# Kernel optimization log

Measured on AMD Instinct MI355X. Metric: run time of the kernel, lower is better.

The kernel has to match this reference:

```python
import jax, jax.numpy as jnp
import numpy as np

N_NODES = 200_000
N_EDGES = 400_000
EMB_DIM = 128
HID_DIM = 24
N_TYPES = 8


def setup_inputs() -> dict:
    key = jax.random.key(0)
    k_emb, k_src, k_typ, k_w1, k_w2 = jax.random.split(key, 5)
    rgcn_emb = jax.random.normal(k_emb, (N_NODES, EMB_DIM), dtype=jnp.float32)
    edge_index = jax.random.randint(k_src, (2, N_EDGES), 0, N_NODES, dtype=jnp.int32)
    edge_type = jax.random.randint(k_typ, (N_EDGES,), 0, N_TYPES, dtype=jnp.int32)
    # per-edge-type 2-layer MLP params: Linear(2D->H), Linear(H->1)
    W1 = jax.random.normal(k_w1, (N_TYPES, 2 * EMB_DIM, HID_DIM), dtype=jnp.float32) * 0.05
    b1 = jnp.zeros((N_TYPES, HID_DIM), dtype=jnp.float32)
    W2 = jax.random.normal(k_w2, (N_TYPES, HID_DIM), dtype=jnp.float32) * 0.05
    b2 = jnp.zeros((N_TYPES,), dtype=jnp.float32)
    return {"rgcn_emb": rgcn_emb, "edge_index": edge_index, "edge_type": edge_type,
            "W1": W1, "b1": b1, "W2": W2, "b2": b2}


def reference(rgcn_emb, edge_index, edge_type, W1, b1, W2, b2):
    src, dst = edge_index[0], edge_index[1]
    # gather + concat: [E, 2D]
    edge_emb = jnp.concatenate([rgcn_emb[src], rgcn_emb[dst]], axis=-1)
    # dense per-type expert compute, then select by routing (MoE-style)
    h = jnp.einsum('ed,tdh->teh', edge_emb, W1) + b1[:, None, :]  # [T,E,H]
    h = jnp.where(h > 0, h, 0.01 * h)  # LeakyReLU(0.01)
    s = jnp.einsum('teh,th->te', h, W2) + b2[:, None]  # [T,E]
    onehot = jax.nn.one_hot(edge_type, N_TYPES, dtype=s.dtype)  # [E,T]
    scores = jnp.einsum('te,et->e', s, onehot)  # scatter-select per edge
    return (scores, rgcn_emb)
```

## Files before the change

kernel.cpp:

```cpp
#include <hip/hip_runtime.h>


typedef float f4 __attribute__((ext_vector_type(4)));

constexpr int N_NODES = 200000;
constexpr int N_EDGES = 400000;
constexpr int EMB_DIM = 128;
constexpr int HID     = 24;
constexpr int N_TYPES = 8;
constexpr int BLK     = 256;

constexpr int CHUNKS  = 128;
constexpr int CH_SZ   = N_EDGES / CHUNKS;
constexpr int MAX_PAD = N_EDGES + N_TYPES * (BLK - 1);
constexpr int SCORE_BLOCKS = (MAX_PAD + BLK - 1) / BLK;
constexpr int COPY_BLOCKS  = 1024;

constexpr int OFF_CC     = 0;
constexpr int OFF_COUNTS = OFF_CC + CHUNKS * N_TYPES;
constexpr int OFF_POFF   = OFF_COUNTS + N_TYPES;
constexpr int OFF_SORTED = OFF_POFF + N_TYPES;
constexpr size_t WS_NEED = (size_t)(OFF_SORTED + MAX_PAD) * sizeof(int);

__global__ __launch_bounds__(BLK) void hist_k(const int* __restrict__ etype,
                                              int* __restrict__ ws) {
    __shared__ int lc[N_TYPES];
    int b = blockIdx.x;
    if (threadIdx.x < N_TYPES) lc[threadIdx.x] = 0;
    __syncthreads();
    int e0 = b * CH_SZ;
    const int4* et4 = (const int4*)(etype + e0);
    for (int e = e0 + (int)threadIdx.x; e < e0 + CH_SZ; e += BLK)
        atomicAdd(&lc[etype[e]], 1);
    (void)et4;
    __syncthreads();
    if (threadIdx.x < N_TYPES)
        ws[OFF_CC + b * N_TYPES + threadIdx.x] = lc[threadIdx.x];
}

__global__ __launch_bounds__(BLK) void scatter_k(
        const int* __restrict__ etype, int* __restrict__ ws) {
    __shared__ int sbase[N_TYPES];
    __shared__ int tot[N_TYPES];
    __shared__ int mybase[N_TYPES];
    __shared__ int spoff[N_TYPES];
    __shared__ int lc[N_TYPES];
    int b = blockIdx.x;
    if (threadIdx.x < N_TYPES) {
        int t = threadIdx.x, s = 0, mb = 0;
        for (int c = 0; c < CHUNKS; ++c) {
            if (c == b) mb = s;
            s += ws[OFF_CC + c * N_TYPES + t];
        }
        tot[t] = s;
        mybase[t] = mb;
        lc[t] = 0;
    }
    __syncthreads();
    if (threadIdx.x == 0) {
        int off = 0;
        for (int t = 0; t < N_TYPES; ++t) {
            spoff[t] = off;
            off += ((tot[t] + BLK - 1) / BLK) * BLK;
        }
    }
    __syncthreads();
    if (threadIdx.x < N_TYPES) {
        sbase[threadIdx.x] = spoff[threadIdx.x] + mybase[threadIdx.x];
        if (b == 0) {
            ws[OFF_COUNTS + threadIdx.x] = tot[threadIdx.x];
            ws[OFF_POFF + threadIdx.x]   = spoff[threadIdx.x];
        }
    }
    __syncthreads();
    int e0 = b * CH_SZ;
    int* sorted = ws + OFF_SORTED;
    for (int e = e0 + (int)threadIdx.x; e < e0 + CH_SZ; e += BLK) {
        int t = etype[e];
        int r = atomicAdd(&lc[t], 1);
        sorted[sbase[t] + r] = e;
    }
}

__device__ __forceinline__ void do_copy(const float* __restrict__ emb,
                                        float* __restrict__ out, int cb, int nb) {
    const f4* s4 = (const f4*)emb;
    f4* o4 = (f4*)(out + N_EDGES);
    const int n4 = N_NODES * EMB_DIM / 4;
    for (int i = cb * BLK + (int)threadIdx.x; i < n4; i += nb * BLK) {
        f4 a = s4[i];
        __builtin_nontemporal_store(a, &o4[i]);
    }
}

__device__ __forceinline__ void half_mm(const f4* __restrict__ x4,
                                        const float* __restrict__ w,
                                        float acc[HID]) {
#pragma unroll 1
    for (int c = 0; c < 4; ++c) {
        f4 r[8];
#pragma unroll
        for (int k = 0; k < 8; ++k) r[k] = x4[c * 8 + k];
#pragma unroll
        for (int k = 0; k < 8; ++k) {
            const float* wp = w + (c * 32 + k * 4) * HID;
#pragma unroll
            for (int j = 0; j < HID; ++j) acc[j] = fmaf(r[k][0], wp[0 * HID + j], acc[j]);
#pragma unroll
            for (int j = 0; j < HID; ++j) acc[j] = fmaf(r[k][1], wp[1 * HID + j], acc[j]);
#pragma unroll
            for (int j = 0; j < HID; ++j) acc[j] = fmaf(r[k][2], wp[2 * HID + j], acc[j]);
#pragma unroll
            for (int j = 0; j < HID; ++j) acc[j] = fmaf(r[k][3], wp[3 * HID + j], acc[j]);
        }
    }
}

__global__ __launch_bounds__(BLK) void score32_k(
        const float* __restrict__ emb,
        const int* __restrict__ srci, const int* __restrict__ dsti,
        const int* __restrict__ ws,
        const float* __restrict__ W1, const float* __restrict__ b1,
        const float* __restrict__ W2, const float* __restrict__ b2,
        float* __restrict__ out) {
    int b = blockIdx.x;
    if (b >= SCORE_BLOCKS) {
        do_copy(emb, out, b - SCORE_BLOCKS, (int)gridDim.x - SCORE_BLOCKS);
        return;
    }
    int poff[N_TYPES], counts[N_TYPES];
#pragma unroll
    for (int t = 0; t < N_TYPES; ++t) {
        counts[t] = ws[OFF_COUNTS + t];
        poff[t]   = ws[OFF_POFF + t];
    }
    int off = poff[N_TYPES - 1] + ((counts[N_TYPES - 1] + BLK - 1) / BLK) * BLK;
    int slot0 = b * BLK;
    if (slot0 >= off) return;
    int t = 0;
#pragma unroll
    for (int i = 1; i < N_TYPES; ++i)
        if (slot0 >= poff[i]) t = i;
    t = __builtin_amdgcn_readfirstlane(t);
    int cnt = counts[t];
    int local = slot0 - poff[t] + (int)threadIdx.x;
    if (local >= cnt) return;
    const int* sorted = ws + OFF_SORTED;
    int e = sorted[slot0 + threadIdx.x];
    int s = srci[e], d = dsti[e];

    float acc[HID];
#pragma unroll
    for (int j = 0; j < HID; ++j) acc[j] = b1[t * HID + j];
    const float* W1t = W1 + (size_t)t * (2 * EMB_DIM * HID);
    half_mm((const f4*)(emb + (size_t)s * EMB_DIM), W1t, acc);
    half_mm((const f4*)(emb + (size_t)d * EMB_DIM), W1t + EMB_DIM * HID, acc);
    float sc = b2[t];
#pragma unroll
    for (int j = 0; j < HID; ++j) {
        float h = acc[j];
        h = (h > 0.f) ? h : 0.01f * h;
        sc = fmaf(h, W2[t * HID + j], sc);
    }
    out[e] = sc;
}

__global__ __launch_bounds__(BLK) void fallback_k(
        const float* __restrict__ emb,
        const int* __restrict__ srci, const int* __restrict__ dsti,
        const int* __restrict__ etype,
        const float* __restrict__ W1, const float* __restrict__ b1,
        const float* __restrict__ W2, const float* __restrict__ b2,
        float* __restrict__ out) {
    long long i0 = (long long)blockIdx.x * BLK + threadIdx.x;
    const f4* s4 = (const f4*)emb;
    f4* o4 = (f4*)(out + N_EDGES);
    const long long n4 = (long long)N_NODES * EMB_DIM / 4;
    for (long long i = i0; i < n4; i += (long long)gridDim.x * BLK)
        o4[i] = s4[i];
    for (int e = (int)i0; e < N_EDGES; e += gridDim.x * BLK) {
        int t = etype[e];
        int s = srci[e], d = dsti[e];
        float acc[HID];
#pragma unroll
        for (int j = 0; j < HID; ++j) acc[j] = b1[t * HID + j];
        const float* w = W1 + (size_t)t * 2 * EMB_DIM * HID;
        half_mm((const f4*)(emb + (size_t)s * EMB_DIM), w, acc);
        half_mm((const f4*)(emb + (size_t)d * EMB_DIM), w + EMB_DIM * HID, acc);
        float sc = b2[t];
#pragma unroll
        for (int j = 0; j < HID; ++j) {
            float h = acc[j];
            h = (h > 0.f) ? h : 0.01f * h;
            sc = fmaf(h, W2[t * HID + j], sc);
        }
        out[e] = sc;
    }
}

extern "C" void kernel_launch(void* const* d_in, const int* in_sizes, int n_in,
                              void* d_out, int out_size, void* d_ws, size_t ws_size,
                              hipStream_t stream) {
    const float* emb   = (const float*)d_in[0];
    const int*   eidx  = (const int*)d_in[1];
    const int*   etype = (const int*)d_in[2];
    const float* W1    = (const float*)d_in[3];
    const float* b1    = (const float*)d_in[4];
    const float* W2    = (const float*)d_in[5];
    const float* b2    = (const float*)d_in[6];
    float* out = (float*)d_out;
    const int* srci = eidx;
    const int* dsti = eidx + N_EDGES;

    if (ws_size >= WS_NEED) {
        int* ws = (int*)d_ws;
        hist_k<<<CHUNKS, BLK, 0, stream>>>(etype, ws);
        scatter_k<<<CHUNKS, BLK, 0, stream>>>(etype, ws);
        score32_k<<<SCORE_BLOCKS + COPY_BLOCKS, BLK, 0, stream>>>(
            emb, srci, dsti, ws, W1, b1, W2, b2, out);
    } else {
        fallback_k<<<2048, BLK, 0, stream>>>(emb, srci, dsti, etype, W1, b1, W2, b2, out);
    }
}
```

Before: 264.2 us.

## Split each edge's src/dst half-matmul across two threads, combine in shared memory

The scoring kernel now handles 128 edges per 256-thread block. The first half of the block multiplies the source embedding against the first half of W1, and the second half multiplies the destination embedding against the second half. Destination partial sums go through a padded shared-memory buffer, and the source threads finish the LeakyReLU and W2 dot product. This doubles thread-level parallelism and halves each thread's serial FMA chain and gather latency, to hide memory latency better. The cost is twice as many score blocks, a block barrier, and shared-memory traffic. The fallback kernel is refactored to use the same 32-column helper.

```diff
diff --git a/kernel.cpp b/kernel.cpp
--- a/kernel.cpp
+++ b/kernel.cpp
@@ -13,7 +13,8 @@
 constexpr int CHUNKS  = 128;
 constexpr int CH_SZ   = N_EDGES / CHUNKS;
 constexpr int MAX_PAD = N_EDGES + N_TYPES * (BLK - 1);
-constexpr int SCORE_BLOCKS = (MAX_PAD + BLK - 1) / BLK;
+constexpr int EPB     = 128;
+constexpr int SCORE_BLOCKS = (MAX_PAD + EPB - 1) / EPB;
 constexpr int COPY_BLOCKS  = 1024;
 
 constexpr int OFF_CC     = 0;
@@ -29,10 +30,8 @@
     if (threadIdx.x < N_TYPES) lc[threadIdx.x] = 0;
     __syncthreads();
     int e0 = b * CH_SZ;
-    const int4* et4 = (const int4*)(etype + e0);
     for (int e = e0 + (int)threadIdx.x; e < e0 + CH_SZ; e += BLK)
         atomicAdd(&lc[etype[e]], 1);
-    (void)et4;
     __syncthreads();
     if (threadIdx.x < N_TYPES)
         ws[OFF_CC + b * N_TYPES + threadIdx.x] = lc[threadIdx.x];
@@ -93,36 +92,31 @@
     }
 }
 
-__device__ __forceinline__ void half_mm(const f4* __restrict__ x4,
-                                        const float* __restrict__ w,
-                                        float acc[HID]) {
-#pragma unroll 1
-    for (int c = 0; c < 4; ++c) {
-        f4 r[8];
-#pragma unroll
-        for (int k = 0; k < 8; ++k) r[k] = x4[c * 8 + k];
-#pragma unroll
-        for (int k = 0; k < 8; ++k) {
-            const float* wp = w + (c * 32 + k * 4) * HID;
-#pragma unroll
-            for (int j = 0; j < HID; ++j) acc[j] = fmaf(r[k][0], wp[0 * HID + j], acc[j]);
-#pragma unroll
-            for (int j = 0; j < HID; ++j) acc[j] = fmaf(r[k][1], wp[1 * HID + j], acc[j]);
-#pragma unroll
-            for (int j = 0; j < HID; ++j) acc[j] = fmaf(r[k][2], wp[2 * HID + j], acc[j]);
-#pragma unroll
-            for (int j = 0; j < HID; ++j) acc[j] = fmaf(r[k][3], wp[3 * HID + j], acc[j]);
-        }
-    }
-}
-
-__global__ __launch_bounds__(BLK) void score32_k(
+__device__ __forceinline__ void cc32(const f4* __restrict__ r,
+                                     const float* __restrict__ w,
+                                     float acc[HID]) {
+#pragma unroll
+    for (int k = 0; k < 8; ++k) {
+        const float* wp = w + (k * 4) * HID;
+#pragma unroll
+        for (int j = 0; j < HID; ++j) acc[j] = fmaf(r[k][0], wp[0 * HID + j], acc[j]);
+#pragma unroll
+        for (int j = 0; j < HID; ++j) acc[j] = fmaf(r[k][1], wp[1 * HID + j], acc[j]);
+#pragma unroll
+        for (int j = 0; j < HID; ++j) acc[j] = fmaf(r[k][2], wp[2 * HID + j], acc[j]);
+#pragma unroll
+        for (int j = 0; j < HID; ++j) acc[j] = fmaf(r[k][3], wp[3 * HID + j], acc[j]);
+    }
+}
+
+__global__ __launch_bounds__(BLK) void score_split_k(
         const float* __restrict__ emb,
         const int* __restrict__ srci, const int* __restrict__ dsti,
         const int* __restrict__ ws,
         const float* __restrict__ W1, const float* __restrict__ b1,
         const float* __restrict__ W2, const float* __restrict__ b2,
         float* __restrict__ out) {
+    __shared__ float jbuf[EPB][HID + 1];
     int b = blockIdx.x;
     if (b >= SCORE_BLOCKS) {
         do_copy(emb, out, b - SCORE_BLOCKS, (int)gridDim.x - SCORE_BLOCKS);
@@ -135,34 +129,54 @@
         poff[t]   = ws[OFF_POFF + t];
     }
     int off = poff[N_TYPES - 1] + ((counts[N_TYPES - 1] + BLK - 1) / BLK) * BLK;
-    int slot0 = b * BLK;
+    int slot0 = b * EPB;
     if (slot0 >= off) return;
     int t = 0;
 #pragma unroll
     for (int i = 1; i < N_TYPES; ++i)
         if (slot0 >= poff[i]) t = i;
     t = __builtin_amdgcn_readfirstlane(t);
-    int cnt = counts[t];
-    int local = slot0 - poff[t] + (int)threadIdx.x;
-    if (local >= cnt) return;
+    const int cnt = counts[t];
+    const int tbase = poff[t];
     const int* sorted = ws + OFF_SORTED;
-    int e = sorted[slot0 + threadIdx.x];
-    int s = srci[e], d = dsti[e];
+
+    const int tid  = (int)threadIdx.x;
+    const int half = __builtin_amdgcn_readfirstlane(tid >> 7);
+    const int idx  = tid & (EPB - 1);
+    const int slot = slot0 + idx;
+    const bool valid = (slot - tbase) < cnt;
+    const int e = sorted[valid ? slot : tbase];
+    const int node = half ? dsti[e] : srci[e];
 
     float acc[HID];
 #pragma unroll
-    for (int j = 0; j < HID; ++j) acc[j] = b1[t * HID + j];
-    const float* W1t = W1 + (size_t)t * (2 * EMB_DIM * HID);
-    half_mm((const f4*)(emb + (size_t)s * EMB_DIM), W1t, acc);
-    half_mm((const f4*)(emb + (size_t)d * EMB_DIM), W1t + EMB_DIM * HID, acc);
-    float sc = b2[t];
-#pragma unroll
-    for (int j = 0; j < HID; ++j) {
-        float h = acc[j];
-        h = (h > 0.f) ? h : 0.01f * h;
-        sc = fmaf(h, W2[t * HID + j], sc);
-    }
-    out[e] = sc;
+    for (int j = 0; j < HID; ++j) acc[j] = half ? 0.f : b1[t * HID + j];
+    const float* Wb = W1 + (size_t)t * (2 * EMB_DIM * HID) + (size_t)half * EMB_DIM * HID;
+    const f4* x = (const f4*)(emb + (size_t)node * EMB_DIM);
+
+    f4 A[8];
+#pragma unroll 1
+    for (int c = 0; c < 4; ++c) {
+#pragma unroll
+        for (int k = 0; k < 8; ++k) A[k] = x[c * 8 + k];
+        cc32(A, Wb + c * 32 * HID, acc);
+    }
+
+    if (half) {
+#pragma unroll
+        for (int j = 0; j < HID; ++j) jbuf[idx][j] = acc[j];
+    }
+    __syncthreads();
+    if (!half && valid) {
+        float sc = b2[t];
+#pragma unroll
+        for (int j = 0; j < HID; ++j) {
+            float h = acc[j] + jbuf[idx][j];
+            h = (h > 0.f) ? h : 0.01f * h;
+            sc = fmaf(h, W2[t * HID + j], sc);
+        }
+        out[e] = sc;
+    }
 }
 
 __global__ __launch_bounds__(BLK) void fallback_k(
@@ -185,8 +199,16 @@
 #pragma unroll
         for (int j = 0; j < HID; ++j) acc[j] = b1[t * HID + j];
         const float* w = W1 + (size_t)t * 2 * EMB_DIM * HID;
-        half_mm((const f4*)(emb + (size_t)s * EMB_DIM), w, acc);
-        half_mm((const f4*)(emb + (size_t)d * EMB_DIM), w + EMB_DIM * HID, acc);
+        const f4* x0 = (const f4*)(emb + (size_t)s * EMB_DIM);
+        const f4* x1 = (const f4*)(emb + (size_t)d * EMB_DIM);
+        f4 A[8];
+#pragma unroll 1
+        for (int c = 0; c < 8; ++c) {
+            const f4* xp = (c < 4) ? x0 : x1;
+#pragma unroll
+            for (int k = 0; k < 8; ++k) A[k] = xp[(c & 3) * 8 + k];
+            cc32(A, w + c * 32 * HID, acc);
+        }
         float sc = b2[t];
 #pragma unroll
         for (int j = 0; j < HID; ++j) {
@@ -216,7 +238,7 @@
         int* ws = (int*)d_ws;
         hist_k<<<CHUNKS, BLK, 0, stream>>>(etype, ws);
         scatter_k<<<CHUNKS, BLK, 0, stream>>>(etype, ws);
-        score32_k<<<SCORE_BLOCKS + COPY_BLOCKS, BLK, 0, stream>>>(
+        score_split_k<<<SCORE_BLOCKS + COPY_BLOCKS, BLK, 0, stream>>>(
             emb, srci, dsti, ws, W1, b1, W2, b2, out);
     } else {
         fallback_k<<<2048, BLK, 0, stream>>>(emb, srci, dsti, etype, W1, b1, W2, b2, out);
```

After: 260.5 us. No clear change (-1.4%).

## Stage gathered embedding rows in LDS and split K across waves per edge tile

Applied to the files above, without the earlier changes.

The scoring kernel now processes 64 edges per 256-thread block. All threads cooperatively gather the src/dst embedding rows into shared memory with coalesced, bank-skewed loads, then each of the four waves computes a quarter of the 128-wide dot product for the same 64 edges. Partial accumulators are reduced through LDS before the activation and output projection. Type buckets are padded to 64 instead of 256. The aim is to replace per-thread uncoalesced row reads with coalesced gathers and to shrink padding waste, at the cost of extra block barriers, LDS traffic and a cross-wave reduction.

```diff
diff --git a/kernel.cpp b/kernel.cpp
--- a/kernel.cpp
+++ b/kernel.cpp
@@ -13,7 +13,10 @@
 constexpr int CHUNKS  = 128;
 constexpr int CH_SZ   = N_EDGES / CHUNKS;
 constexpr int MAX_PAD = N_EDGES + N_TYPES * (BLK - 1);
-constexpr int SCORE_BLOCKS = (MAX_PAD + BLK - 1) / BLK;
+
+constexpr int EB = 64;
+constexpr int MAX_PAD64 = N_EDGES + N_TYPES * (EB - 1);
+constexpr int SCORE_BLOCKS = (MAX_PAD64 + EB - 1) / EB;
 constexpr int COPY_BLOCKS  = 1024;
 
 constexpr int OFF_CC     = 0;
@@ -29,10 +32,8 @@
     if (threadIdx.x < N_TYPES) lc[threadIdx.x] = 0;
     __syncthreads();
     int e0 = b * CH_SZ;
-    const int4* et4 = (const int4*)(etype + e0);
     for (int e = e0 + (int)threadIdx.x; e < e0 + CH_SZ; e += BLK)
         atomicAdd(&lc[etype[e]], 1);
-    (void)et4;
     __syncthreads();
     if (threadIdx.x < N_TYPES)
         ws[OFF_CC + b * N_TYPES + threadIdx.x] = lc[threadIdx.x];
@@ -61,7 +62,7 @@
         int off = 0;
         for (int t = 0; t < N_TYPES; ++t) {
             spoff[t] = off;
-            off += ((tot[t] + BLK - 1) / BLK) * BLK;
+            off += ((tot[t] + EB - 1) / EB) * EB;
         }
     }
     __syncthreads();
@@ -93,36 +94,14 @@
     }
 }
 
-__device__ __forceinline__ void half_mm(const f4* __restrict__ x4,
-                                        const float* __restrict__ w,
-                                        float acc[HID]) {
-#pragma unroll 1
-    for (int c = 0; c < 4; ++c) {
-        f4 r[8];
-#pragma unroll
-        for (int k = 0; k < 8; ++k) r[k] = x4[c * 8 + k];
-#pragma unroll
-        for (int k = 0; k < 8; ++k) {
-            const float* wp = w + (c * 32 + k * 4) * HID;
-#pragma unroll
-            for (int j = 0; j < HID; ++j) acc[j] = fmaf(r[k][0], wp[0 * HID + j], acc[j]);
-#pragma unroll
-            for (int j = 0; j < HID; ++j) acc[j] = fmaf(r[k][1], wp[1 * HID + j], acc[j]);
-#pragma unroll
-            for (int j = 0; j < HID; ++j) acc[j] = fmaf(r[k][2], wp[2 * HID + j], acc[j]);
-#pragma unroll
-            for (int j = 0; j < HID; ++j) acc[j] = fmaf(r[k][3], wp[3 * HID + j], acc[j]);
-        }
-    }
-}
-
-__global__ __launch_bounds__(BLK) void score32_k(
+__global__ __launch_bounds__(BLK) void score_tile_k(
         const float* __restrict__ emb,
         const int* __restrict__ srci, const int* __restrict__ dsti,
         const int* __restrict__ ws,
         const float* __restrict__ W1, const float* __restrict__ b1,
         const float* __restrict__ W2, const float* __restrict__ b2,
         float* __restrict__ out) {
+    __shared__ float lds[EB * EMB_DIM];
     int b = blockIdx.x;
     if (b >= SCORE_BLOCKS) {
         do_copy(emb, out, b - SCORE_BLOCKS, (int)gridDim.x - SCORE_BLOCKS);
@@ -134,35 +113,84 @@
         counts[t] = ws[OFF_COUNTS + t];
         poff[t]   = ws[OFF_POFF + t];
     }
-    int off = poff[N_TYPES - 1] + ((counts[N_TYPES - 1] + BLK - 1) / BLK) * BLK;
-    int slot0 = b * BLK;
+    int off = poff[N_TYPES - 1] + ((counts[N_TYPES - 1] + EB - 1) / EB) * EB;
+    const int slot0 = b * EB;
     if (slot0 >= off) return;
     int t = 0;
 #pragma unroll
     for (int i = 1; i < N_TYPES; ++i)
         if (slot0 >= poff[i]) t = i;
     t = __builtin_amdgcn_readfirstlane(t);
-    int cnt = counts[t];
-    int local = slot0 - poff[t] + (int)threadIdx.x;
-    if (local >= cnt) return;
+    const int cnt = counts[t];
+    const int tbase = poff[t];
     const int* sorted = ws + OFF_SORTED;
-    int e = sorted[slot0 + threadIdx.x];
-    int s = srci[e], d = dsti[e];
+
+    const int tid  = (int)threadIdx.x;
+    const int l    = tid & 63;
+    const int w    = __builtin_amdgcn_readfirstlane(tid >> 6);
+    const int srow = tid >> 5;
+    const int scol = tid & 31;
+    const float* W1t = W1 + (size_t)t * (2 * EMB_DIM * HID);
+    f4* ldsf4 = (f4*)lds;
+    const f4* embf4 = (const f4*)emb;
 
     float acc[HID];
 #pragma unroll
-    for (int j = 0; j < HID; ++j) acc[j] = b1[t * HID + j];
-    const float* W1t = W1 + (size_t)t * (2 * EMB_DIM * HID);
-    half_mm((const f4*)(emb + (size_t)s * EMB_DIM), W1t, acc);
-    half_mm((const f4*)(emb + (size_t)d * EMB_DIM), W1t + EMB_DIM * HID, acc);
-    float sc = b2[t];
-#pragma unroll
-    for (int j = 0; j < HID; ++j) {
-        float h = acc[j];
-        h = (h > 0.f) ? h : 0.01f * h;
-        sc = fmaf(h, W2[t * HID + j], sc);
-    }
-    out[e] = sc;
+    for (int j = 0; j < HID; ++j) acc[j] = 0.f;
+
+#pragma unroll 1
+    for (int phase = 0; phase < 2; ++phase) {
+        const int* __restrict__ nodes = phase ? dsti : srci;
+        if (phase) __syncthreads();
+#pragma unroll
+        for (int j = 0; j < 8; ++j) {
+            int row  = j * 8 + srow;
+            int slot = slot0 + row;
+            int e    = sorted[((slot - tbase) < cnt) ? slot : tbase];
+            int nd   = nodes[e];
+            ldsf4[row * 32 + ((scol + row) & 31)] = embf4[(size_t)nd * 32 + scol];
+        }
+        __syncthreads();
+        const float* wp0 = W1t + (size_t)(phase * EMB_DIM + w * 32) * HID;
+#pragma unroll
+        for (int k = 0; k < 8; ++k) {
+            int C = w * 8 + k;
+            f4 rv = ldsf4[l * 32 + ((C + l) & 31)];
+            const float* wp = wp0 + (k * 4) * HID;
+#pragma unroll
+            for (int j = 0; j < HID; ++j) acc[j] = fmaf(rv[0], wp[0 * HID + j], acc[j]);
+#pragma unroll
+            for (int j = 0; j < HID; ++j) acc[j] = fmaf(rv[1], wp[1 * HID + j], acc[j]);
+#pragma unroll
+            for (int j = 0; j < HID; ++j) acc[j] = fmaf(rv[2], wp[2 * HID + j], acc[j]);
+#pragma unroll
+            for (int j = 0; j < HID; ++j) acc[j] = fmaf(rv[3], wp[3 * HID + j], acc[j]);
+        }
+    }
+
+    __syncthreads();
+    if (w != 0) {
+#pragma unroll
+        for (int j = 0; j < HID; ++j) lds[(l * 4 + w) * 25 + j] = acc[j];
+    }
+    __syncthreads();
+    if (w == 0) {
+        int slot = slot0 + l;
+        if ((slot - tbase) < cnt) {
+            int e = sorted[slot];
+            float sc = b2[t];
+#pragma unroll
+            for (int j = 0; j < HID; ++j) {
+                float h = acc[j] + lds[(l * 4 + 1) * 25 + j]
+                                 + lds[(l * 4 + 2) * 25 + j]
+                                 + lds[(l * 4 + 3) * 25 + j]
+                                 + b1[t * HID + j];
+                h = (h > 0.f) ? h : 0.01f * h;
+                sc = fmaf(h, W2[t * HID + j], sc);
+            }
+            out[e] = sc;
+        }
+    }
 }
 
 __global__ __launch_bounds__(BLK) void fallback_k(
@@ -184,9 +212,17 @@
         float acc[HID];
 #pragma unroll
         for (int j = 0; j < HID; ++j) acc[j] = b1[t * HID + j];
-        const float* w = W1 + (size_t)t * 2 * EMB_DIM * HID;
-        half_mm((const f4*)(emb + (size_t)s * EMB_DIM), w, acc);
-        half_mm((const f4*)(emb + (size_t)d * EMB_DIM), w + EMB_DIM * HID, acc);
+        const float* wb = W1 + (size_t)t * 2 * EMB_DIM * HID;
+        for (int k = 0; k < EMB_DIM; ++k) {
+            float x = emb[(size_t)s * EMB_DIM + k];
+#pragma unroll
+            for (int j = 0; j < HID; ++j) acc[j] = fmaf(x, wb[k * HID + j], acc[j]);
+        }
+        for (int k = 0; k < EMB_DIM; ++k) {
+            float x = emb[(size_t)d * EMB_DIM + k];
+#pragma unroll
+            for (int j = 0; j < HID; ++j) acc[j] = fmaf(x, wb[(EMB_DIM + k) * HID + j], acc[j]);
+        }
         float sc = b2[t];
 #pragma unroll
         for (int j = 0; j < HID; ++j) {
@@ -216,7 +252,7 @@
         int* ws = (int*)d_ws;
         hist_k<<<CHUNKS, BLK, 0, stream>>>(etype, ws);
         scatter_k<<<CHUNKS, BLK, 0, stream>>>(etype, ws);
-        score32_k<<<SCORE_BLOCKS + COPY_BLOCKS, BLK, 0, stream>>>(
+        score_tile_k<<<SCORE_BLOCKS + COPY_BLOCKS, BLK, 0, stream>>>(
             emb, srci, dsti, ws, W1, b1, W2, b2, out);
     } else {
         fallback_k<<<2048, BLK, 0, stream>>>(emb, srci, dsti, etype, W1, b1, W2, b2, out);
```

Result: slower. 327.8 us (+24.0%).

## Compute per-type edge MLP with fp16 MFMA over 64-edge groups

Applied to the files above, without the earlier changes.

Replaces the per-thread scalar FP32 dot products with MFMA 16x16x32 fp16 matrix ops. Each wave handles 16 edges and each block handles 4 groups of 64 type-sorted edges, so the padding granularity drops from 256 to 64. W1 fragments are converted to fp16 and kept in registers, and are reloaded only when the type changes. This removes the FMA-bound inner loop and the heavy W1 reads per thread, at the cost of fp16 rounding on the embeddings and weights.

```diff
diff --git a/kernel.cpp b/kernel.cpp
--- a/kernel.cpp
+++ b/kernel.cpp
@@ -1,7 +1,9 @@
 #include <hip/hip_runtime.h>
 
 
-typedef float f4 __attribute__((ext_vector_type(4)));
+typedef float    f4   __attribute__((ext_vector_type(4)));
+typedef _Float16 h8   __attribute__((ext_vector_type(8)));
+typedef float    f32x4 __attribute__((ext_vector_type(4)));
 
 constexpr int N_NODES = 200000;
 constexpr int N_EDGES = 400000;
@@ -13,8 +15,13 @@
 constexpr int CHUNKS  = 128;
 constexpr int CH_SZ   = N_EDGES / CHUNKS;
 constexpr int MAX_PAD = N_EDGES + N_TYPES * (BLK - 1);
-constexpr int SCORE_BLOCKS = (MAX_PAD + BLK - 1) / BLK;
-constexpr int COPY_BLOCKS  = 1024;
+
+constexpr int EB        = 64;
+constexpr int MAX_PAD64 = N_EDGES + N_TYPES * (EB - 1);
+constexpr int NGRP      = (MAX_PAD64 + EB - 1) / EB;
+constexpr int GPB       = 4;
+constexpr int SCORE_MB  = (NGRP + GPB - 1) / GPB;
+constexpr int COPY_BLOCKS = 1024;
 
 constexpr int OFF_CC     = 0;
 constexpr int OFF_COUNTS = OFF_CC + CHUNKS * N_TYPES;
@@ -29,10 +36,8 @@
     if (threadIdx.x < N_TYPES) lc[threadIdx.x] = 0;
     __syncthreads();
     int e0 = b * CH_SZ;
-    const int4* et4 = (const int4*)(etype + e0);
     for (int e = e0 + (int)threadIdx.x; e < e0 + CH_SZ; e += BLK)
         atomicAdd(&lc[etype[e]], 1);
-    (void)et4;
     __syncthreads();
     if (threadIdx.x < N_TYPES)
         ws[OFF_CC + b * N_TYPES + threadIdx.x] = lc[threadIdx.x];
@@ -61,7 +66,7 @@
         int off = 0;
         for (int t = 0; t < N_TYPES; ++t) {
             spoff[t] = off;
-            off += ((tot[t] + BLK - 1) / BLK) * BLK;
+            off += ((tot[t] + EB - 1) / EB) * EB;
         }
     }
     __syncthreads();
@@ -93,30 +98,7 @@
     }
 }
 
-__device__ __forceinline__ void half_mm(const f4* __restrict__ x4,
-                                        const float* __restrict__ w,
-                                        float acc[HID]) {
-#pragma unroll 1
-    for (int c = 0; c < 4; ++c) {
-        f4 r[8];
-#pragma unroll
-        for (int k = 0; k < 8; ++k) r[k] = x4[c * 8 + k];
-#pragma unroll
-        for (int k = 0; k < 8; ++k) {
-            const float* wp = w + (c * 32 + k * 4) * HID;
-#pragma unroll
-            for (int j = 0; j < HID; ++j) acc[j] = fmaf(r[k][0], wp[0 * HID + j], acc[j]);
-#pragma unroll
-            for (int j = 0; j < HID; ++j) acc[j] = fmaf(r[k][1], wp[1 * HID + j], acc[j]);
-#pragma unroll
-            for (int j = 0; j < HID; ++j) acc[j] = fmaf(r[k][2], wp[2 * HID + j], acc[j]);
-#pragma unroll
-            for (int j = 0; j < HID; ++j) acc[j] = fmaf(r[k][3], wp[3 * HID + j], acc[j]);
-        }
-    }
-}
-
-__global__ __launch_bounds__(BLK) void score32_k(
+__global__ __launch_bounds__(BLK) void score_mfma_k(
         const float* __restrict__ emb,
         const int* __restrict__ srci, const int* __restrict__ dsti,
         const int* __restrict__ ws,
@@ -124,8 +106,8 @@
         const float* __restrict__ W2, const float* __restrict__ b2,
         float* __restrict__ out) {
     int b = blockIdx.x;
-    if (b >= SCORE_BLOCKS) {
-        do_copy(emb, out, b - SCORE_BLOCKS, (int)gridDim.x - SCORE_BLOCKS);
+    if (b >= SCORE_MB) {
+        do_copy(emb, out, b - SCORE_MB, (int)gridDim.x - SCORE_MB);
         return;
     }
     int poff[N_TYPES], counts[N_TYPES];
@@ -134,35 +116,102 @@
         counts[t] = ws[OFF_COUNTS + t];
         poff[t]   = ws[OFF_POFF + t];
     }
-    int off = poff[N_TYPES - 1] + ((counts[N_TYPES - 1] + BLK - 1) / BLK) * BLK;
-    int slot0 = b * BLK;
-    if (slot0 >= off) return;
-    int t = 0;
-#pragma unroll
-    for (int i = 1; i < N_TYPES; ++i)
-        if (slot0 >= poff[i]) t = i;
-    t = __builtin_amdgcn_readfirstlane(t);
-    int cnt = counts[t];
-    int local = slot0 - poff[t] + (int)threadIdx.x;
-    if (local >= cnt) return;
+    const int off = poff[N_TYPES - 1]
+                  + ((counts[N_TYPES - 1] + EB - 1) / EB) * EB;
     const int* sorted = ws + OFF_SORTED;
-    int e = sorted[slot0 + threadIdx.x];
-    int s = srci[e], d = dsti[e];
-
-    float acc[HID];
-#pragma unroll
-    for (int j = 0; j < HID; ++j) acc[j] = b1[t * HID + j];
-    const float* W1t = W1 + (size_t)t * (2 * EMB_DIM * HID);
-    half_mm((const f4*)(emb + (size_t)s * EMB_DIM), W1t, acc);
-    half_mm((const f4*)(emb + (size_t)d * EMB_DIM), W1t + EMB_DIM * HID, acc);
-    float sc = b2[t];
-#pragma unroll
-    for (int j = 0; j < HID; ++j) {
-        float h = acc[j];
-        h = (h > 0.f) ? h : 0.01f * h;
-        sc = fmaf(h, W2[t * HID + j], sc);
-    }
-    out[e] = sc;
+
+    const int tid = (int)threadIdx.x;
+    const int l   = tid & 63;
+    const int w   = tid >> 6;
+    const int lm  = l & 15;
+    const int lg  = l >> 4;
+
+    h8 wf[16];
+    float b1v0[4], w2v0[4], b1v1[4], w2v1[4];
+    float b2t = 0.f;
+    int cur_t = -1, tbase = 0, cnt = 0;
+
+#pragma unroll 1
+    for (int g = b * GPB; g < (b + 1) * GPB && g < NGRP; ++g) {
+        const int slot0g = g * EB;
+        if (slot0g >= off) break;
+        int t = 0;
+#pragma unroll
+        for (int i = 1; i < N_TYPES; ++i)
+            if (slot0g >= poff[i]) t = i;
+        t = __builtin_amdgcn_readfirstlane(t);
+        if (t != cur_t) {
+            cur_t = t;
+            tbase = poff[t];
+            cnt   = counts[t];
+            const float* W1t = W1 + (size_t)t * (2 * EMB_DIM * HID);
+#pragma unroll
+            for (int s = 0; s < 8; ++s) {
+#pragma unroll
+                for (int m = 0; m < 2; ++m) {
+                    const int colh = m * 16 + lm;
+                    const float* wp = W1t + (size_t)(32 * s + lg * 8) * HID + colh;
+                    h8 f;
+                    if (colh < HID) {
+#pragma unroll
+                        for (int i = 0; i < 8; ++i) f[i] = (_Float16)wp[i * HID];
+                    } else {
+#pragma unroll
+                        for (int i = 0; i < 8; ++i) f[i] = (_Float16)0.f;
+                    }
+                    wf[s * 2 + m] = f;
+                }
+            }
+#pragma unroll
+            for (int i = 0; i < 4; ++i) {
+                const int j0 = lg * 4 + i;
+                b1v0[i] = b1[t * HID + j0];
+                w2v0[i] = W2[t * HID + j0];
+                const int j1 = 16 + j0;
+                const bool v1 = j1 < HID;
+                b1v1[i] = v1 ? b1[t * HID + j1] : 0.f;
+                w2v1[i] = v1 ? W2[t * HID + j1] : 0.f;
+            }
+            b2t = b2[t];
+        }
+        if (cnt == 0) continue;
+        const int slot_w = slot0g + w * 16;
+        const int slot   = slot_w + lm;
+        const bool evalid = (slot - tbase) < cnt;
+        const int e  = sorted[evalid ? slot : tbase];
+        const int ns = srci[e], nd = dsti[e];
+
+        f32x4 acc0 = {0.f, 0.f, 0.f, 0.f};
+        f32x4 acc1 = {0.f, 0.f, 0.f, 0.f};
+#pragma unroll
+        for (int s = 0; s < 8; ++s) {
+            const float* xr = emb + (size_t)(s < 4 ? ns : nd) * EMB_DIM
+                            + (s & 3) * 32 + lg * 8;
+            f4 lo = *(const f4*)xr;
+            f4 hi = *(const f4*)(xr + 4);
+            h8 xb;
+            xb[0] = (_Float16)lo[0]; xb[1] = (_Float16)lo[1];
+            xb[2] = (_Float16)lo[2]; xb[3] = (_Float16)lo[3];
+            xb[4] = (_Float16)hi[0]; xb[5] = (_Float16)hi[1];
+            xb[6] = (_Float16)hi[2]; xb[7] = (_Float16)hi[3];
+            acc0 = __builtin_amdgcn_mfma_f32_16x16x32_f16(wf[s * 2 + 0], xb, acc0, 0, 0, 0);
+            acc1 = __builtin_amdgcn_mfma_f32_16x16x32_f16(wf[s * 2 + 1], xb, acc1, 0, 0, 0);
+        }
+        float v = 0.f;
+#pragma unroll
+        for (int i = 0; i < 4; ++i) {
+            float h0 = acc0[i] + b1v0[i];
+            h0 = (h0 > 0.f) ? h0 : 0.01f * h0;
+            v = fmaf(h0, w2v0[i], v);
+            float h1 = acc1[i] + b1v1[i];
+            h1 = (h1 > 0.f) ? h1 : 0.01f * h1;
+            v = fmaf(h1, w2v1[i], v);
+        }
+        v += __shfl_xor(v, 16);
+        v += __shfl_xor(v, 32);
+        if (l < 16 && evalid)
+            out[e] = v + b2t;
+    }
 }
 
 __global__ __launch_bounds__(BLK) void fallback_k(
@@ -184,9 +233,17 @@
         float acc[HID];
 #pragma unroll
         for (int j = 0; j < HID; ++j) acc[j] = b1[t * HID + j];
-        const float* w = W1 + (size_t)t * 2 * EMB_DIM * HID;
-        half_mm((const f4*)(emb + (size_t)s * EMB_DIM), w, acc);
-        half_mm((const f4*)(emb + (size_t)d * EMB_DIM), w + EMB_DIM * HID, acc);
+        const float* wb = W1 + (size_t)t * 2 * EMB_DIM * HID;
+        for (int k = 0; k < EMB_DIM; ++k) {
+            float x = emb[(size_t)s * EMB_DIM + k];
+#pragma unroll
+            for (int j = 0; j < HID; ++j) acc[j] = fmaf(x, wb[k * HID + j], acc[j]);
+        }
+        for (int k = 0; k < EMB_DIM; ++k) {
+            float x = emb[(size_t)d * EMB_DIM + k];
+#pragma unroll
+            for (int j = 0; j < HID; ++j) acc[j] = fmaf(x, wb[(EMB_DIM + k) * HID + j], acc[j]);
+        }
         float sc = b2[t];
 #pragma unroll
         for (int j = 0; j < HID; ++j) {
@@ -216,7 +273,7 @@
         int* ws = (int*)d_ws;
         hist_k<<<CHUNKS, BLK, 0, stream>>>(etype, ws);
         scatter_k<<<CHUNKS, BLK, 0, stream>>>(etype, ws);
-        score32_k<<<SCORE_BLOCKS + COPY_BLOCKS, BLK, 0, stream>>>(
+        score_mfma_k<<<SCORE_MB + COPY_BLOCKS, BLK, 0, stream>>>(
             emb, srci, dsti, ws, W1, b1, W2, b2, out);
     } else {
         fallback_k<<<2048, BLK, 0, stream>>>(emb, srci, dsti, etype, W1, b1, W2, b2, out);
```

Result: slower. 272.5 us (+3.1%).
